# Optimization experiments

Hardware: AMD Instinct MI355X
Metric: run time of the kernel (lower is better)

The kernel has to match this reference:

```python
import jax, jax.numpy as jnp
import numpy as np

B, K, E, L, H, ENS = 32768, 5, 16, 128, 3, 3

def setup_inputs() -> dict:
    key = jax.random.key(0)
    ks = jax.random.split(key, 16)
    w = lambda i, shape: (jax.random.normal(ks[i], shape, jnp.float32) * 0.05)
    return {
        "z": jax.random.normal(ks[0], (B, L), jnp.float32),
        "anchors": jax.random.normal(ks[1], (B, K, 2), jnp.float32),
        # anchor_embed MLP: Linear(2,E) -> ReLU -> Linear(E,E)
        "W1": w(2, (E, 2)), "b1": w(3, (E,)),
        "W2": w(4, (E, E)), "b2": w(5, (E,)),
        # LSTMCell(E, L): gates order i,f,g,o
        "W_ih": w(6, (4 * L, E)), "W_hh": w(7, (4 * L, L)),
        "b_ih": w(8, (4 * L,)), "b_hh": w(9, (4 * L,)),
        # progress head Linear(L,1)
        "Wp": w(10, (1, L)), "bp": w(11, (1,)),
        # risk ensemble: ENS stacked Linear(L,1)
        "Wr": w(12, (ENS, L)), "br": w(13, (ENS,)),
    }

def reference(z, anchors, W1, b1, W2, b2, W_ih, W_hh, b_ih, b_hh, Wp, bp, Wr, br):
    Bc, Kc, _ = anchors.shape
    # anchor embedding MLP (B,K,2) -> (B,K,E)
    emb = jnp.maximum(anchors @ W1.T + b1, 0.0) @ W2.T + b2
    inp = emb.reshape(Bc * Kc, -1)                      # (B*K, E)
    h = jnp.broadcast_to(z[:, None, :], (Bc, Kc, z.shape[-1])).reshape(Bc * Kc, -1)
    c = jnp.zeros_like(h)
    x_proj = inp @ W_ih.T + b_ih                        # input projection constant over steps
    for _ in range(H):  # fixed small rollout horizon
        gates = x_proj + h @ W_hh.T + b_hh              # (B*K, 4L)
        i_g, f_g, g_g, o_g = jnp.split(gates, 4, axis=-1)
        i_g = jax.nn.sigmoid(i_g)
        f_g = jax.nn.sigmoid(f_g)
        g_g = jnp.tanh(g_g)
        o_g = jax.nn.sigmoid(o_g)
        c = f_g * c + i_g * g_g
        h = o_g * jnp.tanh(c)
    h = h.reshape(Bc, Kc, -1)                           # (B,K,L)
    progress = (h @ Wp.T + bp)[..., 0]                  # (B,K)
    risks = jnp.einsum('bkl,el->ebk', h, Wr) + br[:, None, None]  # (ENS,B,K)
    risk_mean = risks.mean(axis=0)
    unc = jnp.var(jax.nn.sigmoid(risks), axis=0, ddof=1)  # torch .var is unbiased
    return risk_mean, progress, unc, risks
```

## Files before the change

kernel.cpp:

```cpp
#include <hip/hip_runtime.h>

#define BN 32768
#define KN 5
#define LN 128
#define EN 16
#define HN 3
#define ROWS (BN*KN)
#define BK (BN*KN)
#define MT 32
#define TILES (ROWS/MT)
#define WGS 512
#define TPW (TILES/WGS)
#define THREADS 512
#define ASTR 168
#define HSTR 132

using bf16x8 = __attribute__((ext_vector_type(8))) __bf16;
using f32x4  = __attribute__((ext_vector_type(4))) float;
using u16x8  = __attribute__((ext_vector_type(8))) unsigned short;

__device__ inline unsigned short f2bf(float x) {
    union { float f; unsigned u; } v; v.f = x;
    unsigned r = v.u + 0x7FFFu + ((v.u >> 16) & 1u);
    return (unsigned short)(r >> 16);
}
__device__ inline float sigm(float x) {
    return __builtin_amdgcn_rcpf(1.0f + __builtin_amdgcn_exp2f(-1.44269504089f * x));
}
__device__ inline float tanh_(float x) {
    return 1.0f - 2.0f * __builtin_amdgcn_rcpf(1.0f + __builtin_amdgcn_exp2f(2.88539008178f * x));
}
__device__ inline f32x4 splat4(float x) { f32x4 r; r[0]=x; r[1]=x; r[2]=x; r[3]=x; return r; }

__global__ __launch_bounds__(THREADS, 2)
void wahead_kernel(const float* __restrict__ z,   const float* __restrict__ anchors,
                   const float* __restrict__ W1,  const float* __restrict__ b1,
                   const float* __restrict__ W2,  const float* __restrict__ b2,
                   const float* __restrict__ Wih, const float* __restrict__ Whh,
                   const float* __restrict__ bih, const float* __restrict__ bhh,
                   const float* __restrict__ Wp,  const float* __restrict__ bp,
                   const float* __restrict__ Wr,  const float* __restrict__ br,
                   float* __restrict__ out)
{
    __shared__ unsigned short sA[2 * MT * ASTR];
    __shared__ float sHf[MT * HSTR];
    __shared__ float sW1[32], sb1[16], sW2[256], sb2[16], sWp[128], sWr[384];

    const int tid  = threadIdx.x;
    const int wv   = tid >> 6;
    const int lane = tid & 63;
    const int quad = lane >> 4;
    const int cc   = lane & 15;

    if (tid < 32)  sW1[tid] = W1[tid];
    if (tid < 16)  { sb1[tid] = b1[tid]; sb2[tid] = b2[tid]; }
    if (tid < 256) sW2[tid] = W2[tid];
    if (tid < 128) sWp[tid] = Wp[tid];
    if (tid < 384) sWr[tid] = Wr[tid];

    bf16x8 Bf[4][5];
    float biasv[4];
    #pragma unroll
    for (int t = 0; t < 4; ++t) {
        const int n = t * 128 + wv * 16 + cc;
        biasv[t] = bih[n] + bhh[n];
        #pragma unroll
        for (int kt = 0; kt < 5; ++kt) {
            const int k0 = kt * 32 + quad * 8;
            float v[8];
            if (k0 < 16) {
                const float4 p0 = *reinterpret_cast<const float4*>(Wih + n * 16 + k0);
                const float4 p1 = *reinterpret_cast<const float4*>(Wih + n * 16 + k0 + 4);
                v[0]=p0.x; v[1]=p0.y; v[2]=p0.z; v[3]=p0.w;
                v[4]=p1.x; v[5]=p1.y; v[6]=p1.z; v[7]=p1.w;
            } else if (k0 < 144) {
                const float4 p0 = *reinterpret_cast<const float4*>(Whh + n * 128 + (k0 - 16));
                const float4 p1 = *reinterpret_cast<const float4*>(Whh + n * 128 + (k0 - 16) + 4);
                v[0]=p0.x; v[1]=p0.y; v[2]=p0.z; v[3]=p0.w;
                v[4]=p1.x; v[5]=p1.y; v[6]=p1.z; v[7]=p1.w;
            } else {
                #pragma unroll
                for (int j = 0; j < 8; ++j) v[j] = 0.0f;
            }
            union { bf16x8 bv; unsigned short us[8]; } pk;
            #pragma unroll
            for (int j = 0; j < 8; ++j) pk.us[j] = f2bf(v[j]);
            Bf[t][kt] = pk.bv;
        }
    }

    const float bpv = bp[0];
    const float br0 = br[0], br1 = br[1], br2 = br[2];

    __syncthreads();

    const int erow = tid >> 4;
    const int esub = tid & 15;

    for (int ti = 0; ti < TPW; ++ti) {
        const int tile = blockIdx.x * TPW + ti;
        const int r0g  = tile * MT;

        {
            const int gr = r0g + erow;
            const float ax = anchors[gr * 2], ay = anchors[gr * 2 + 1];
            float acc_e = sb2[esub];
            #pragma unroll
            for (int hh = 0; hh < 16; ++hh) {
                float pre = fmaf(sW1[hh * 2], ax, fmaf(sW1[hh * 2 + 1], ay, sb1[hh]));
                pre = fmaxf(pre, 0.0f);
                acc_e = fmaf(pre, sW2[esub * 16 + hh], acc_e);
            }
            const unsigned short eb = f2bf(acc_e);
            sA[0 * MT * ASTR + erow * ASTR + esub] = eb;
            sA[1 * MT * ASTR + erow * ASTR + esub] = eb;
            sA[0 * MT * ASTR + erow * ASTR + 144 + esub] = 0;
            sA[1 * MT * ASTR + erow * ASTR + 144 + esub] = 0;
            const unsigned b_idx = (unsigned)gr / 5u;
            const float4* zp = reinterpret_cast<const float4*>(z + (size_t)b_idx * 128 + esub * 8);
            const float4 z0 = zp[0], z1 = zp[1];
            union { u16x8 v; unsigned short us[8]; } zz;
            zz.us[0]=f2bf(z0.x); zz.us[1]=f2bf(z0.y); zz.us[2]=f2bf(z0.z); zz.us[3]=f2bf(z0.w);
            zz.us[4]=f2bf(z1.x); zz.us[5]=f2bf(z1.y); zz.us[6]=f2bf(z1.z); zz.us[7]=f2bf(z1.w);
            *reinterpret_cast<u16x8*>(&sA[0 * MT * ASTR + erow * ASTR + 16 + esub * 8]) = zz.v;
        }

        float cst[2][4] = {{0,0,0,0},{0,0,0,0}};

        #pragma unroll
        for (int s = 0; s < HN; ++s) {
            const int cur = s & 1;
            const int nxt = cur ^ 1;
            __syncthreads();

            f32x4 acc[2][4];
            #pragma unroll
            for (int mt = 0; mt < 2; ++mt)
                #pragma unroll
                for (int t = 0; t < 4; ++t)
                    acc[mt][t] = splat4(biasv[t]);

            #pragma unroll
            for (int kt = 0; kt < 5; ++kt) {
                const bf16x8 a0 = *reinterpret_cast<const bf16x8*>(
                    &sA[cur * MT * ASTR + cc * ASTR + kt * 32 + quad * 8]);
                const bf16x8 a1 = *reinterpret_cast<const bf16x8*>(
                    &sA[cur * MT * ASTR + (16 + cc) * ASTR + kt * 32 + quad * 8]);
                #pragma unroll
                for (int t = 0; t < 4; ++t) {
                    acc[0][t] = __builtin_amdgcn_mfma_f32_16x16x32_bf16(a0, Bf[t][kt], acc[0][t], 0, 0, 0);
                    acc[1][t] = __builtin_amdgcn_mfma_f32_16x16x32_bf16(a1, Bf[t][kt], acc[1][t], 0, 0, 0);
                }
            }

            const int lcol = wv * 16 + cc;
            #pragma unroll
            for (int mt = 0; mt < 2; ++mt) {
                #pragma unroll
                for (int r = 0; r < 4; ++r) {
                    const float ig = sigm(acc[mt][0][r]);
                    const float fg = sigm(acc[mt][1][r]);
                    const float gg = tanh_(acc[mt][2][r]);
                    const float og = sigm(acc[mt][3][r]);
                    const float cn = fmaf(fg, cst[mt][r], ig * gg);
                    cst[mt][r] = cn;
                    const float hn = og * tanh_(cn);
                    const int m = mt * 16 + quad * 4 + r;
                    if (s == HN - 1) {
                        sHf[m * HSTR + lcol] = hn;
                    } else {
                        sA[nxt * MT * ASTR + m * ASTR + 16 + lcol] = f2bf(hn);
                    }
                }
            }
        }

        __syncthreads();

        {
            const int row = tid >> 4;
            const int j   = tid & 15;
            float p = 0.f, q0 = 0.f, q1 = 0.f, q2 = 0.f;
            #pragma unroll
            for (int u = 0; u < 8; ++u) {
                const int l = j * 8 + u;
                const float hv = sHf[row * HSTR + l];
                p  = fmaf(hv, sWp[l], p);
                q0 = fmaf(hv, sWr[l], q0);
                q1 = fmaf(hv, sWr[128 + l], q1);
                q2 = fmaf(hv, sWr[256 + l], q2);
            }
            #pragma unroll
            for (int m = 1; m < 16; m <<= 1) {
                p  += __shfl_xor(p,  m, 64);
                q0 += __shfl_xor(q0, m, 64);
                q1 += __shfl_xor(q1, m, 64);
                q2 += __shfl_xor(q2, m, 64);
            }
            if (j == 0) {
                const int gr = r0g + row;
                const float prog  = p + bpv;
                const float rr0 = q0 + br0, rr1 = q1 + br1, rr2 = q2 + br2;
                const float rmean = (rr0 + rr1 + rr2) * (1.0f / 3.0f);
                const float s0 = sigm(rr0), s1 = sigm(rr1), s2 = sigm(rr2);
                const float sm = (s0 + s1 + s2) * (1.0f / 3.0f);
                const float d0 = s0 - sm, d1 = s1 - sm, d2 = s2 - sm;
                const float unc = (d0 * d0 + d1 * d1 + d2 * d2) * 0.5f;
                out[gr]          = rmean;
                out[BK + gr]     = prog;
                out[2 * BK + gr] = unc;
                out[3 * BK + gr] = rr0;
                out[4 * BK + gr] = rr1;
                out[5 * BK + gr] = rr2;
            }
        }
    }
}

extern "C" void kernel_launch(void* const* d_in, const int* in_sizes, int n_in,
                              void* d_out, int out_size, void* d_ws, size_t ws_size,
                              hipStream_t stream) {
    const float* z       = (const float*)d_in[0];
    const float* anchors = (const float*)d_in[1];
    const float* W1      = (const float*)d_in[2];
    const float* b1      = (const float*)d_in[3];
    const float* W2      = (const float*)d_in[4];
    const float* b2      = (const float*)d_in[5];
    const float* Wih     = (const float*)d_in[6];
    const float* Whh     = (const float*)d_in[7];
    const float* bih     = (const float*)d_in[8];
    const float* bhh     = (const float*)d_in[9];
    const float* Wp      = (const float*)d_in[10];
    const float* bp      = (const float*)d_in[11];
    const float* Wr      = (const float*)d_in[12];
    const float* br      = (const float*)d_in[13];

    hipLaunchKernelGGL(wahead_kernel, dim3(WGS), dim3(THREADS), 0, stream,
                       z, anchors, W1, b1, W2, b2, Wih, Whh, bih, bhh,
                       Wp, bp, Wr, br, (float*)d_out);
}
```

Baseline: 236.6 us.

## Prepack scaled bf16 LSTM weights to workspace and stream them from L2

Adds a prepack kernel that converts W_ih/W_hh to bf16 in MFMA fragment order, pre-scaled by log2e factors so the gate activations become raw exp2 calls. The main kernel no longer holds the 20 weight fragments in registers; it reloads them from global/L2 each step with double-buffered prefetch, which allows 4 workgroups per CU instead of 2. The LSTM cell update is rewritten algebraically to use fewer reciprocals. The final hidden state is kept in bf16 in the shared A buffer rather than a separate fp32 array, and the W2 shared-memory layout is padded. The cost is extra global traffic for weights on every step, an extra kernel launch, and reduced precision of the final h used for the heads.

```diff
diff --git a/kernel.cpp b/kernel.cpp
--- a/kernel.cpp
+++ b/kernel.cpp
@@ -3,19 +3,19 @@
 #define BN 32768
 #define KN 5
 #define LN 128
-#define EN 16
 #define HN 3
 #define ROWS (BN*KN)
-#define BK (BN*KN)
+#define BK ROWS
 #define MT 32
 #define TILES (ROWS/MT)
 #define WGS 512
 #define TPW (TILES/WGS)
 #define THREADS 512
 #define ASTR 168
-#define HSTR 132
+#define LOG2E 1.44269504089f
 
 using bf16x8 = __attribute__((ext_vector_type(8))) __bf16;
+using bf16x2 = __attribute__((ext_vector_type(2))) __bf16;
 using f32x4  = __attribute__((ext_vector_type(4))) float;
 using u16x8  = __attribute__((ext_vector_type(8))) unsigned short;
 
@@ -24,27 +24,59 @@
     unsigned r = v.u + 0x7FFFu + ((v.u >> 16) & 1u);
     return (unsigned short)(r >> 16);
 }
+#if __has_builtin(__builtin_amdgcn_cvt_pk_bf16_f32)
+__device__ inline unsigned short f2bf_fast(float x) {
+    union { bf16x2 v; unsigned short us[2]; } u;
+    u.v = __builtin_amdgcn_cvt_pk_bf16_f32(x, x);
+    return u.us[0];
+}
+#else
+__device__ inline unsigned short f2bf_fast(float x) { return f2bf(x); }
+#endif
+__device__ inline float bf2f(unsigned short b) {
+    union { unsigned u; float f; } v; v.u = ((unsigned)b) << 16; return v.f;
+}
 __device__ inline float sigm(float x) {
-    return __builtin_amdgcn_rcpf(1.0f + __builtin_amdgcn_exp2f(-1.44269504089f * x));
-}
-__device__ inline float tanh_(float x) {
-    return 1.0f - 2.0f * __builtin_amdgcn_rcpf(1.0f + __builtin_amdgcn_exp2f(2.88539008178f * x));
+    return __builtin_amdgcn_rcpf(1.0f + __builtin_amdgcn_exp2f(-LOG2E * x));
 }
 __device__ inline f32x4 splat4(float x) { f32x4 r; r[0]=x; r[1]=x; r[2]=x; r[3]=x; return r; }
 
-__global__ __launch_bounds__(THREADS, 2)
+__global__ __launch_bounds__(256)
+void prepack_kernel(const float* __restrict__ Wih, const float* __restrict__ Whh,
+                    uint4* __restrict__ Bpk)
+{
+    const int gid  = blockIdx.x * 256 + threadIdx.x;
+    const int lane = gid & 63;
+    const int w    = gid >> 6;
+    const int wv   = w & 7;
+    const int t    = (w >> 3) & 3;
+    const int kt   = w >> 5;
+    const float sc = (t == 2) ? (2.0f * LOG2E) : (-LOG2E);
+    const int n  = t * 128 + wv * 16 + (lane & 15);
+    const int k0 = kt * 32 + (lane >> 4) * 8;
+    union { uint4 u; unsigned short us[8]; } pk;
+    #pragma unroll
+    for (int j = 0; j < 8; ++j) {
+        const int ks = k0 + j;
+        float v = 0.0f;
+        if (ks < 16)       v = Wih[n * 16 + ks];
+        else if (ks < 144) v = Whh[n * 128 + (ks - 16)];
+        pk.us[j] = f2bf(sc * v);
+    }
+    Bpk[gid] = pk.u;
+}
+
+__global__ __launch_bounds__(THREADS, 4)
 void wahead_kernel(const float* __restrict__ z,   const float* __restrict__ anchors,
                    const float* __restrict__ W1,  const float* __restrict__ b1,
                    const float* __restrict__ W2,  const float* __restrict__ b2,
-                   const float* __restrict__ Wih, const float* __restrict__ Whh,
                    const float* __restrict__ bih, const float* __restrict__ bhh,
                    const float* __restrict__ Wp,  const float* __restrict__ bp,
                    const float* __restrict__ Wr,  const float* __restrict__ br,
-                   float* __restrict__ out)
+                   const uint4* __restrict__ Bpk, float* __restrict__ out)
 {
     __shared__ unsigned short sA[2 * MT * ASTR];
-    __shared__ float sHf[MT * HSTR];
-    __shared__ float sW1[32], sb1[16], sW2[256], sb2[16], sWp[128], sWr[384];
+    __shared__ float sW1[32], sb1[16], sW2[16 * 17], sb2[16], sWp[128], sWr[384];
 
     const int tid  = threadIdx.x;
     const int wv   = tid >> 6;
@@ -54,49 +86,28 @@
 
     if (tid < 32)  sW1[tid] = W1[tid];
     if (tid < 16)  { sb1[tid] = b1[tid]; sb2[tid] = b2[tid]; }
-    if (tid < 256) sW2[tid] = W2[tid];
+    if (tid < 256) sW2[(tid >> 4) * 17 + (tid & 15)] = W2[tid];
     if (tid < 128) sWp[tid] = Wp[tid];
     if (tid < 384) sWr[tid] = Wr[tid];
 
-    bf16x8 Bf[4][5];
     float biasv[4];
     #pragma unroll
     for (int t = 0; t < 4; ++t) {
+        const float sc = (t == 2) ? (2.0f * LOG2E) : (-LOG2E);
         const int n = t * 128 + wv * 16 + cc;
-        biasv[t] = bih[n] + bhh[n];
-        #pragma unroll
-        for (int kt = 0; kt < 5; ++kt) {
-            const int k0 = kt * 32 + quad * 8;
-            float v[8];
-            if (k0 < 16) {
-                const float4 p0 = *reinterpret_cast<const float4*>(Wih + n * 16 + k0);
-                const float4 p1 = *reinterpret_cast<const float4*>(Wih + n * 16 + k0 + 4);
-                v[0]=p0.x; v[1]=p0.y; v[2]=p0.z; v[3]=p0.w;
-                v[4]=p1.x; v[5]=p1.y; v[6]=p1.z; v[7]=p1.w;
-            } else if (k0 < 144) {
-                const float4 p0 = *reinterpret_cast<const float4*>(Whh + n * 128 + (k0 - 16));
-                const float4 p1 = *reinterpret_cast<const float4*>(Whh + n * 128 + (k0 - 16) + 4);
-                v[0]=p0.x; v[1]=p0.y; v[2]=p0.z; v[3]=p0.w;
-                v[4]=p1.x; v[5]=p1.y; v[6]=p1.z; v[7]=p1.w;
-            } else {
-                #pragma unroll
-                for (int j = 0; j < 8; ++j) v[j] = 0.0f;
-            }
-            union { bf16x8 bv; unsigned short us[8]; } pk;
-            #pragma unroll
-            for (int j = 0; j < 8; ++j) pk.us[j] = f2bf(v[j]);
-            Bf[t][kt] = pk.bv;
-        }
+        biasv[t] = sc * (bih[n] + bhh[n]);
     }
-
     const float bpv = bp[0];
     const float br0 = br[0], br1 = br[1], br2 = br[2];
 
+    const uint4* Bw = Bpk + wv * 64 + lane;
+
     __syncthreads();
 
     const int erow = tid >> 4;
     const int esub = tid & 15;
 
+    #pragma unroll 1
     for (int ti = 0; ti < TPW; ++ti) {
         const int tile = blockIdx.x * TPW + ti;
         const int r0g  = tile * MT;
@@ -109,7 +120,7 @@
             for (int hh = 0; hh < 16; ++hh) {
                 float pre = fmaf(sW1[hh * 2], ax, fmaf(sW1[hh * 2 + 1], ay, sb1[hh]));
                 pre = fmaxf(pre, 0.0f);
-                acc_e = fmaf(pre, sW2[esub * 16 + hh], acc_e);
+                acc_e = fmaf(pre, sW2[esub * 17 + hh], acc_e);
             }
             const unsigned short eb = f2bf(acc_e);
             sA[0 * MT * ASTR + erow * ASTR + esub] = eb;
@@ -122,10 +133,12 @@
             union { u16x8 v; unsigned short us[8]; } zz;
             zz.us[0]=f2bf(z0.x); zz.us[1]=f2bf(z0.y); zz.us[2]=f2bf(z0.z); zz.us[3]=f2bf(z0.w);
             zz.us[4]=f2bf(z1.x); zz.us[5]=f2bf(z1.y); zz.us[6]=f2bf(z1.z); zz.us[7]=f2bf(z1.w);
-            *reinterpret_cast<u16x8*>(&sA[0 * MT * ASTR + erow * ASTR + 16 + esub * 8]) = zz.v;
+            *reinterpret_cast<u16x8*>(&sA[erow * ASTR + 16 + esub * 8]) = zz.v;
         }
 
-        float cst[2][4] = {{0,0,0,0},{0,0,0,0}};
+        float cst[8];
+        #pragma unroll
+        for (int e = 0; e < 8; ++e) cst[e] = 0.0f;
 
         #pragma unroll
         for (int s = 0; s < HN; ++s) {
@@ -140,38 +153,52 @@
                 for (int t = 0; t < 4; ++t)
                     acc[mt][t] = splat4(biasv[t]);
 
+            union { uint4 u; bf16x8 b; } Bb[2][4];
+            bf16x8 Ab[2][2];
+            #pragma unroll
+            for (int t = 0; t < 4; ++t) Bb[0][t].u = Bw[t * 512];
+            #pragma unroll
+            for (int mt = 0; mt < 2; ++mt)
+                Ab[0][mt] = *reinterpret_cast<const bf16x8*>(
+                    &sA[cur * MT * ASTR + (mt * 16 + cc) * ASTR + quad * 8]);
+
             #pragma unroll
             for (int kt = 0; kt < 5; ++kt) {
-                const bf16x8 a0 = *reinterpret_cast<const bf16x8*>(
-                    &sA[cur * MT * ASTR + cc * ASTR + kt * 32 + quad * 8]);
-                const bf16x8 a1 = *reinterpret_cast<const bf16x8*>(
-                    &sA[cur * MT * ASTR + (16 + cc) * ASTR + kt * 32 + quad * 8]);
+                const int cb = kt & 1, nb = cb ^ 1;
+                if (kt < 4) {
+                    #pragma unroll
+                    for (int t = 0; t < 4; ++t) Bb[nb][t].u = Bw[((kt + 1) * 4 + t) * 512];
+                    #pragma unroll
+                    for (int mt = 0; mt < 2; ++mt)
+                        Ab[nb][mt] = *reinterpret_cast<const bf16x8*>(
+                            &sA[cur * MT * ASTR + (mt * 16 + cc) * ASTR + (kt + 1) * 32 + quad * 8]);
+                }
                 #pragma unroll
                 for (int t = 0; t < 4; ++t) {
-                    acc[0][t] = __builtin_amdgcn_mfma_f32_16x16x32_bf16(a0, Bf[t][kt], acc[0][t], 0, 0, 0);
-                    acc[1][t] = __builtin_amdgcn_mfma_f32_16x16x32_bf16(a1, Bf[t][kt], acc[1][t], 0, 0, 0);
+                    acc[0][t] = __builtin_amdgcn_mfma_f32_16x16x32_bf16(Ab[cb][0], Bb[cb][t].b, acc[0][t], 0, 0, 0);
+                    acc[1][t] = __builtin_amdgcn_mfma_f32_16x16x32_bf16(Ab[cb][1], Bb[cb][t].b, acc[1][t], 0, 0, 0);
                 }
             }
 
             const int lcol = wv * 16 + cc;
             #pragma unroll
-            for (int mt = 0; mt < 2; ++mt) {
-                #pragma unroll
-                for (int r = 0; r < 4; ++r) {
-                    const float ig = sigm(acc[mt][0][r]);
-                    const float fg = sigm(acc[mt][1][r]);
-                    const float gg = tanh_(acc[mt][2][r]);
-                    const float og = sigm(acc[mt][3][r]);
-                    const float cn = fmaf(fg, cst[mt][r], ig * gg);
-                    cst[mt][r] = cn;
-                    const float hn = og * tanh_(cn);
-                    const int m = mt * 16 + quad * 4 + r;
-                    if (s == HN - 1) {
-                        sHf[m * HSTR + lcol] = hn;
-                    } else {
-                        sA[nxt * MT * ASTR + m * ASTR + 16 + lcol] = f2bf(hn);
-                    }
-                }
+            for (int e = 0; e < 8; ++e) {
+                const int mt = e >> 2, r = e & 3;
+                const float Ei = __builtin_amdgcn_exp2f(acc[mt][0][r]);
+                const float Ef = __builtin_amdgcn_exp2f(acc[mt][1][r]);
+                const float Eg = __builtin_amdgcn_exp2f(acc[mt][2][r]);
+                const float Eo = __builtin_amdgcn_exp2f(acc[mt][3][r]);
+                const float t1  = (1.0f + Ei) * (1.0f + Eg);
+                const float ef1 = 1.0f + Ef;
+                const float t3  = (Eg - 1.0f) * ef1;
+                const float num = fmaf(cst[e], t1, t3);
+                const float cn  = num * __builtin_amdgcn_rcpf(t1 * ef1);
+                cst[e] = cn;
+                const float Ec = __builtin_amdgcn_exp2f(2.0f * LOG2E * cn);
+                const float hn = (Ec - 1.0f) *
+                    __builtin_amdgcn_rcpf((1.0f + Eo) * (1.0f + Ec));
+                const int m = mt * 16 + quad * 4 + r;
+                sA[nxt * MT * ASTR + m * ASTR + 16 + lcol] = f2bf_fast(hn);
             }
         }
 
@@ -180,11 +207,13 @@
         {
             const int row = tid >> 4;
             const int j   = tid & 15;
+            const u16x8 hv8 = *reinterpret_cast<const u16x8*>(
+                &sA[1 * MT * ASTR + row * ASTR + 16 + j * 8]);
             float p = 0.f, q0 = 0.f, q1 = 0.f, q2 = 0.f;
             #pragma unroll
             for (int u = 0; u < 8; ++u) {
                 const int l = j * 8 + u;
-                const float hv = sHf[row * HSTR + l];
+                const float hv = bf2f(hv8[u]);
                 p  = fmaf(hv, sWp[l], p);
                 q0 = fmaf(hv, sWr[l], q0);
                 q1 = fmaf(hv, sWr[128 + l], q1);
@@ -235,7 +264,10 @@
     const float* Wr      = (const float*)d_in[12];
     const float* br      = (const float*)d_in[13];
 
+    uint4* Bpk = (uint4*)d_ws;
+
+    hipLaunchKernelGGL(prepack_kernel, dim3(40), dim3(256), 0, stream, Wih, Whh, Bpk);
     hipLaunchKernelGGL(wahead_kernel, dim3(WGS), dim3(THREADS), 0, stream,
-                       z, anchors, W1, b1, W2, b2, Wih, Whh, bih, bhh,
-                       Wp, bp, Wr, br, (float*)d_out);
-}
+                       z, anchors, W1, b1, W2, b2, bih, bhh,
+                       Wp, bp, Wr, br, (const uint4*)Bpk, (float*)d_out);
+}
```

Measured after the change: 404.9 us. 1.71x slower.
